# Kernel optimization log

Hardware: AMD Instinct MI355X
Metric: run time of the kernel (lower is better)

## Reference

```python
import jax, jax.numpy as jnp
import numpy as np

N, D_IN, F = 65536, 512, 256
E = 524288
BATCH, K1 = 32, 200
BN_EPS = 1e-5


def setup_inputs() -> dict:
    key = jax.random.key(0)
    ks = iter(jax.random.split(key, 64))

    def nrm(shape, s=0.05):
        return jax.random.normal(next(ks), shape, jnp.float32) * s

    inp = {
        "feat": jax.random.normal(next(ks), (N, D_IN), jnp.float32),
        "A": jax.random.randint(next(ks), (2, E), 0, N, dtype=jnp.int32),
        "h1id": jax.random.randint(next(ks), (BATCH * K1,), 0, N // BATCH, dtype=jnp.int32),
        "batch": BATCH,
    }
    dims = [(D_IN, F), (F, F), (F, F), (F, F)]
    for i, (di, do) in enumerate(dims, 1):
        inp[f"eps{i}"] = jnp.zeros((), jnp.float32)          # GINConv train_eps, init 0
        inp[f"w{i}a"] = nrm((di, do)); inp[f"b{i}a"] = jnp.zeros((do,), jnp.float32)
        inp[f"w{i}b"] = nrm((do, do)); inp[f"b{i}b"] = jnp.zeros((do,), jnp.float32)
        inp[f"g{i}"] = jnp.ones((do,), jnp.float32)          # BN gamma
        inp[f"be{i}"] = jnp.zeros((do,), jnp.float32)        # BN beta
        inp[f"m{i}"] = nrm((do,))                            # BN running mean
        inp[f"v{i}"] = jax.random.uniform(next(ks), (do,), jnp.float32, 0.5, 1.5)  # BN running var
    inp["wc1"] = nrm((F, F)); inp["bc1"] = jnp.zeros((F,), jnp.float32)
    inp["pa"] = jnp.full((F,), 0.25, jnp.float32)            # PReLU per-channel slope
    inp["wc2"] = nrm((F, 2)); inp["bc2"] = jnp.zeros((2,), jnp.float32)
    return inp


def _gin_conv(x, src, dst, eps, wa, ba, wb, bb, g, be, m, v):
    # sum aggregation over in-edges: aggr[i] = sum_{(j->i)} x[j]
    aggr = jax.ops.segment_sum(x[src], dst, num_segments=N)
    h = (1.0 + eps) * x + aggr
    h = jax.nn.relu(h @ wa + ba) @ wb + bb
    # BatchNorm1d in eval mode (running stats)
    return (h - m) * jax.lax.rsqrt(v + BN_EPS) * g + be


def _forward(feat, A, h1id, batch,
             eps1, w1a, b1a, w1b, b1b, g1, be1, m1, v1,
             eps2, w2a, b2a, w2b, b2b, g2, be2, m2, v2,
             eps3, w3a, b3a, w3b, b3b, g3, be3, m3, v3,
             eps4, w4a, b4a, w4b, b4b, g4, be4, m4, v4,
             wc1, bc1, pa, wc2, bc2):
    src, dst = A[0], A[1]
    h = jax.nn.relu(_gin_conv(feat, src, dst, eps1, w1a, b1a, w1b, b1b, g1, be1, m1, v1))
    h = jax.nn.relu(_gin_conv(h, src, dst, eps2, w2a, b2a, w2b, b2b, g2, be2, m2, v2))
    h = jax.nn.relu(_gin_conv(h, src, dst, eps3, w3a, b3a, w3b, b3b, g3, be3, m3, v3))
    h = _gin_conv(h, src, dst, eps4, w4a, b4a, w4b, b4b, g4, be4, m4, v4)
    score = h.reshape(batch, -1, F)                      # [B, n_per_graph, F]
    idx = h1id.reshape(batch, K1)
    edge_feat = jnp.take_along_axis(score, idx[:, :, None], axis=1)  # [B, K1, F]
    ef = edge_feat.reshape(-1, F)
    hc = ef @ wc1 + bc1
    hc = jnp.where(hc > 0, hc, pa * hc)                  # PReLU(256)
    return hc @ wc2 + bc2                                # [B*K1, 2]


def reference(feat, A, h1id, batch,
              eps1, w1a, b1a, w1b, b1b, g1, be1, m1, v1,
              eps2, w2a, b2a, w2b, b2b, g2, be2, m2, v2,
              eps3, w3a, b3a, w3b, b3b, g3, be3, m3, v3,
              eps4, w4a, b4a, w4b, b4b, g4, be4, m4, v4,
              wc1, bc1, pa, wc2, bc2):
    return _forward(feat, A, h1id, batch,
                    eps1, w1a, b1a, w1b, b1b, g1, be1, m1, v1,
                    eps2, w2a, b2a, w2b, b2b, g2, be2, m2, v2,
                    eps3, w3a, b3a, w3b, b3b, g3, be3, m3, v3,
                    eps4, w4a, b4a, w4b, b4b, g4, be4, m4, v4,
                    wc1, bc1, pa, wc2, bc2)
```

## Files before the change

kernel.cpp:

```cpp
#include <hip/hip_runtime.h>

typedef unsigned short u16;
typedef unsigned int   u32;
typedef __bf16  bf16x8 __attribute__((ext_vector_type(8)));
typedef float   f32x4  __attribute__((ext_vector_type(4)));
typedef u32     u32x4  __attribute__((ext_vector_type(4)));

#define NN 65536
#define NE 524288
#define FD 256

typedef const __attribute__((address_space(1))) void* gas_p;
typedef __attribute__((address_space(3))) void* las_p;
#define GLDS16(g, l) __builtin_amdgcn_global_load_lds((gas_p)(const void*)(g), (las_p)(void*)(l), 16, 0, 0)

__device__ __forceinline__ u16 f2bf(float f){
  u32 u = __float_as_uint(f);
  u += 0x7fffu + ((u >> 16) & 1u);
  return (u16)(u >> 16);
}
__device__ __forceinline__ float bf2f(u32 lo16){
  return __uint_as_float(lo16 << 16);
}
__device__ __forceinline__ void acc8(float* a, uint4 v){
  a[0] += bf2f(v.x & 0xffffu); a[1] += bf2f(v.x >> 16);
  a[2] += bf2f(v.y & 0xffffu); a[3] += bf2f(v.y >> 16);
  a[4] += bf2f(v.z & 0xffffu); a[5] += bf2f(v.z >> 16);
  a[6] += bf2f(v.w & 0xffffu); a[7] += bf2f(v.w >> 16);
}
__device__ __forceinline__ int lsw(int row, int c){
  return row * 256 + ((((c >> 3) ^ (row & 7)) & 31) << 3) + (c & 7);
}

__global__ __launch_bounds__(256) void prep_hist_k(
    const float* __restrict__ w1a, const float* __restrict__ w1b,
    const float* __restrict__ w2a, const float* __restrict__ w2b,
    const float* __restrict__ w3a, const float* __restrict__ w3b,
    const float* __restrict__ w4a, const float* __restrict__ w4b,
    const float* __restrict__ wc1, u16* __restrict__ wT,
    const int* __restrict__ dst, int* __restrict__ deg)
{
  if (blockIdx.x >= 2560){
    int e = (blockIdx.x - 2560) * 256 + threadIdx.x;
    atomicAdd(&deg[dst[e]], 1);
    return;
  }
  int idx = blockIdx.x * 256 + threadIdx.x;
  const float* src; int base, K, local;
  if (idx < 131072){ src = w1a; base = 0; K = 512; local = idx; }
  else {
    local = idx - 131072;
    int j = local >> 16;
    local &= 65535;
    K = 256;
    base = 131072 + j * 65536;
    switch (j){
      case 0: src = w1b; break;
      case 1: src = w2a; break;
      case 2: src = w2b; break;
      case 3: src = w3a; break;
      case 4: src = w3b; break;
      case 5: src = w4a; break;
      case 6: src = w4b; break;
      default: src = wc1; break;
    }
  }
  int n = local & 255;
  int k = local >> 8;
  wT[base + n * K + k] = f2bf(src[k * 256 + n]);
}

__global__ __launch_bounds__(1024) void scan_k(const int* __restrict__ deg, int* __restrict__ rs){
  __shared__ int part[1024];
  int t = threadIdx.x;
  int base = t * 64;
  int sum = 0;
  for (int i = 0; i < 64; ++i) sum += deg[base + i];
  part[t] = sum;
  __syncthreads();
  for (int off = 1; off < 1024; off <<= 1){
    int v = 0;
    if (t >= off) v = part[t - off];
    __syncthreads();
    part[t] += v;
    __syncthreads();
  }
  int run = part[t] - sum;
  for (int i = 0; i < 64; ++i){ rs[base + i] = run; run += deg[base + i]; }
  if (t == 1023) rs[65536] = part[1023];
}

__global__ __launch_bounds__(256) void scat_k(
    const int* __restrict__ src, const int* __restrict__ dst,
    const int* __restrict__ rs, int* __restrict__ cursor, int* __restrict__ csr)
{
  int e = blockIdx.x * 256 + threadIdx.x;
  int d = dst[e];
  int pos = atomicAdd(&cursor[d], 1);
  csr[rs[d] + pos] = src[e];
}

template<int AF32, int MODE, int RELU, int K>
__global__ __launch_bounds__(512) void gemm_k(
    const void* __restrict__ Ap, const u16* __restrict__ Bt,
    u16* __restrict__ C,
    const float* __restrict__ p0, const float* __restrict__ p1,
    const float* __restrict__ p2, const float* __restrict__ p3,
    const float* __restrict__ p4)
{
  __shared__ u16 lds[32768];
  u16* As = lds;
  u16* Bs = lds + 8192;
  const int t    = threadIdx.x;
  const int lane = t & 63;
  const int w    = t >> 6;
  const int wm   = w & 1;
  const int wn   = w >> 1;
  const int m0   = blockIdx.x * 128;
  const int mrow = lane & 15;
  const int quad = lane >> 4;

  f32x4 acc[4][4];
  const f32x4 zero = {0.f, 0.f, 0.f, 0.f};
  #pragma unroll
  for (int i = 0; i < 4; ++i)
    #pragma unroll
    for (int j = 0; j < 4; ++j) acc[i][j] = zero;

  const u16* Ab = (const u16*)Ap;
  const float* Af = (const float*)Ap;

  for (int k0 = 0; k0 < K; k0 += 64){
    if (AF32){
      #pragma unroll
      for (int i = 0; i < 2; ++i){
        int p   = i * 512 + t;
        int row = p >> 3;
        const float* s = Af + (size_t)(m0 + row) * K + k0 + (p & 7) * 8;
        float4 x0 = *(const float4*)s;
        float4 x1 = *(const float4*)(s + 4);
        union { u32x4 q; u16 h[8]; } u;
        u.h[0] = f2bf(x0.x); u.h[1] = f2bf(x0.y); u.h[2] = f2bf(x0.z); u.h[3] = f2bf(x0.w);
        u.h[4] = f2bf(x1.x); u.h[5] = f2bf(x1.y); u.h[6] = f2bf(x1.z); u.h[7] = f2bf(x1.w);
        int dst = (p & ~7) | ((p & 7) ^ (row & 7));
        *(u32x4*)&As[dst * 8] = u.q;
      }
    } else {
      #pragma unroll
      for (int i = 0; i < 2; ++i){
        int p   = i * 512 + t;
        int row = p >> 3;
        int ch  = (p & 7) ^ (row & 7);
        GLDS16(Ab + (size_t)(m0 + row) * K + k0 + ch * 8, &As[p * 8]);
      }
    }
    #pragma unroll
    for (int i = 0; i < 4; ++i){
      int p   = i * 512 + t;
      int row = p >> 3;
      int ch  = (p & 7) ^ (row & 7);
      GLDS16(Bt + (size_t)row * K + k0 + ch * 8, &Bs[p * 8]);
    }
    __syncthreads();
    #pragma unroll
    for (int ks = 0; ks < 2; ++ks){
      bf16x8 af[4], bq[4];
      #pragma unroll
      for (int mi = 0; mi < 4; ++mi){
        int r  = wm * 64 + mi * 16 + mrow;
        int ch = (quad + ks * 4) ^ (r & 7);
        af[mi] = *(const bf16x8*)&As[(r * 8 + ch) * 8];
      }
      #pragma unroll
      for (int ni = 0; ni < 4; ++ni){
        int rb = wn * 64 + ni * 16 + mrow;
        int ch = (quad + ks * 4) ^ (rb & 7);
        bq[ni] = *(const bf16x8*)&Bs[(rb * 8 + ch) * 8];
      }
      #pragma unroll
      for (int mi = 0; mi < 4; ++mi)
        #pragma unroll
        for (int ni = 0; ni < 4; ++ni)
          acc[mi][ni] = __builtin_amdgcn_mfma_f32_16x16x32_bf16(af[mi], bq[ni], acc[mi][ni], 0, 0, 0);
    }
    __syncthreads();
  }

  #pragma unroll
  for (int ni = 0; ni < 4; ++ni){
    int c  = wn * 64 + ni * 16 + mrow;
    float scale = 1.f, shift = 0.f;
    if (MODE == 1){
      float s = p0[c] * rsqrtf(p3[c] + 1e-5f);
      scale = s;
      shift = (p4[c] - p2[c]) * s + p1[c];
    }
    #pragma unroll
    for (int mi = 0; mi < 4; ++mi){
      int rbase = wm * 64 + mi * 16 + quad * 4;
      #pragma unroll
      for (int reg = 0; reg < 4; ++reg){
        float v = acc[mi][ni][reg];
        if (MODE == 1){
          v = v * scale + shift;
          if (RELU) v = fmaxf(v, 0.f);
        }
        lds[lsw(rbase + reg, c)] = f2bf(v);
      }
    }
  }
  __syncthreads();
  #pragma unroll
  for (int i = 0; i < 8; ++i){
    int p  = i * 512 + t;
    int r  = p >> 5;
    int ch = p & 31;
    u32x4 q = *(const u32x4*)&lds[r * 256 + (ch ^ (r & 7)) * 8];
    *(u32x4*)&C[(size_t)(m0 + r) * 256 + ch * 8] = q;
  }
}

template<int GATH, int RAW>
__global__ __launch_bounds__(256) void agg_k(
    const u16* __restrict__ y, const int* __restrict__ rs, const int* __restrict__ csr,
    const float* __restrict__ epsp, const float* __restrict__ bias,
    const int* __restrict__ gidx, u16* __restrict__ tout)
{
  int sub    = threadIdx.x >> 5;
  int lane32 = threadIdx.x & 31;
  int idx    = blockIdx.x * 8 + sub;
  int node;
  if (GATH) node = (idx / 200) * 2048 + gidx[idx];
  else      node = idx;
  int f0 = lane32 * 8;
  float e1 = 1.0f + epsp[0];
  int s0 = rs[node], s1 = rs[node + 1];
  uint4 own = *(const uint4*)(y + (size_t)node * 256 + f0);
  float a[8] = {0.f,0.f,0.f,0.f,0.f,0.f,0.f,0.f};
  int e = s0;
  for (; e + 4 <= s1; e += 4){
    int sa = csr[e], sb = csr[e+1], sc = csr[e+2], sd = csr[e+3];
    uint4 va = *(const uint4*)(y + (size_t)sa * 256 + f0);
    uint4 vb = *(const uint4*)(y + (size_t)sb * 256 + f0);
    uint4 vc = *(const uint4*)(y + (size_t)sc * 256 + f0);
    uint4 vd = *(const uint4*)(y + (size_t)sd * 256 + f0);
    acc8(a, va); acc8(a, vb); acc8(a, vc); acc8(a, vd);
  }
  for (; e < s1; ++e){
    int s = csr[e];
    acc8(a, *(const uint4*)(y + (size_t)s * 256 + f0));
  }
  float ow[8];
  ow[0] = bf2f(own.x & 0xffffu); ow[1] = bf2f(own.x >> 16);
  ow[2] = bf2f(own.y & 0xffffu); ow[3] = bf2f(own.y >> 16);
  ow[4] = bf2f(own.z & 0xffffu); ow[5] = bf2f(own.z >> 16);
  ow[6] = bf2f(own.w & 0xffffu); ow[7] = bf2f(own.w >> 16);
  float r[8];
  if (RAW){
    #pragma unroll
    for (int q = 0; q < 8; ++q) r[q] = e1 * ow[q] + a[q];
  } else {
    float4 b0 = *(const float4*)(bias + f0);
    float4 b1 = *(const float4*)(bias + f0 + 4);
    r[0] = fmaxf(e1 * ow[0] + a[0] + b0.x, 0.f);
    r[1] = fmaxf(e1 * ow[1] + a[1] + b0.y, 0.f);
    r[2] = fmaxf(e1 * ow[2] + a[2] + b0.z, 0.f);
    r[3] = fmaxf(e1 * ow[3] + a[3] + b0.w, 0.f);
    r[4] = fmaxf(e1 * ow[4] + a[4] + b1.x, 0.f);
    r[5] = fmaxf(e1 * ow[5] + a[5] + b1.y, 0.f);
    r[6] = fmaxf(e1 * ow[6] + a[6] + b1.z, 0.f);
    r[7] = fmaxf(e1 * ow[7] + a[7] + b1.w, 0.f);
  }
  uint4 o;
  o.x = (u32)f2bf(r[0]) | ((u32)f2bf(r[1]) << 16);
  o.y = (u32)f2bf(r[2]) | ((u32)f2bf(r[3]) << 16);
  o.z = (u32)f2bf(r[4]) | ((u32)f2bf(r[5]) << 16);
  o.w = (u32)f2bf(r[6]) | ((u32)f2bf(r[7]) << 16);
  *(uint4*)(tout + (size_t)idx * 256 + f0) = o;
}

__global__ __launch_bounds__(512) void tail_k(
    const u16* __restrict__ u4p, const u16* __restrict__ w4aT, const float* __restrict__ ba4,
    const u16* __restrict__ w4bT,
    const float* __restrict__ g, const float* __restrict__ be,
    const float* __restrict__ m, const float* __restrict__ v,
    const float* __restrict__ bb,
    const u16* __restrict__ wc1T, const float* __restrict__ bc1, const float* __restrict__ pa,
    const float* __restrict__ wc2, const float* __restrict__ bc2,
    float* __restrict__ out)
{
  __shared__ u16 lds[32768];
  const int t    = threadIdx.x;
  const int lane = t & 63;
  const int w    = t >> 6;
  const int wm   = w & 1;
  const int wn   = w >> 1;
  const int m0   = blockIdx.x * 128;
  const int mrow = lane & 15;
  const int quad = lane >> 4;
  const f32x4 zero = {0.f, 0.f, 0.f, 0.f};

  #pragma unroll
  for (int i = 0; i < 8; ++i){
    int p   = i * 512 + t;
    int row = p >> 5;
    int ch  = (p & 31) ^ (row & 7);
    GLDS16(u4p + (size_t)(m0 + row) * 256 + ch * 8, &lds[p * 8]);
  }
  __syncthreads();

  #pragma unroll 1
  for (int stage = 0; stage < 3; ++stage){
    const u16* Bt = (stage == 0) ? w4aT : (stage == 1) ? w4bT : wc1T;
    f32x4 acc[4][4];
    #pragma unroll
    for (int i = 0; i < 4; ++i)
      #pragma unroll
      for (int j = 0; j < 4; ++j) acc[i][j] = zero;
    #pragma unroll
    for (int ks = 0; ks < 8; ++ks){
      bf16x8 af[4], bq[4];
      #pragma unroll
      for (int mi = 0; mi < 4; ++mi){
        int r    = wm * 64 + mi * 16 + mrow;
        int slot = (ks * 4 + quad) ^ (r & 7);
        af[mi] = *(const bf16x8*)&lds[r * 256 + slot * 8];
      }
      #pragma unroll
      for (int ni = 0; ni < 4; ++ni){
        int rb = wn * 64 + ni * 16 + mrow;
        bq[ni] = *(const bf16x8*)&Bt[(size_t)rb * 256 + ks * 32 + quad * 8];
      }
      #pragma unroll
      for (int mi = 0; mi < 4; ++mi)
        #pragma unroll
        for (int ni = 0; ni < 4; ++ni)
          acc[mi][ni] = __builtin_amdgcn_mfma_f32_16x16x32_bf16(af[mi], bq[ni], acc[mi][ni], 0, 0, 0);
    }
    __syncthreads();
    #pragma unroll
    for (int ni = 0; ni < 4; ++ni){
      int c = wn * 64 + ni * 16 + mrow;
      float scale = 1.f, shift = 0.f, slope = 0.f; int prelu = 0, rel = 0;
      if (stage == 0){ shift = ba4[c]; rel = 1; }
      if (stage == 1){
        float s = g[c] * rsqrtf(v[c] + 1e-5f);
        scale = s;
        shift = (bb[c] - m[c]) * s + be[c];
      }
      if (stage == 2){ shift = bc1[c]; slope = pa[c]; prelu = 1; }
      #pragma unroll
      for (int mi = 0; mi < 4; ++mi){
        int rbase = wm * 64 + mi * 16 + quad * 4;
        #pragma unroll
        for (int reg = 0; reg < 4; ++reg){
          float val = acc[mi][ni][reg] * scale + shift;
          if (rel)   val = fmaxf(val, 0.f);
          if (prelu) val = val > 0.f ? val : slope * val;
          lds[lsw(rbase + reg, c)] = f2bf(val);
        }
      }
    }
    __syncthreads();
  }

  {
    int c0 = lane * 4;
    float4 wva = *(const float4*)(wc2 + c0 * 2);
    float4 wvb = *(const float4*)(wc2 + c0 * 2 + 4);
    float o0 = bc2[0], o1 = bc2[1];
    #pragma unroll 1
    for (int rr = 0; rr < 16; ++rr){
      int row = w * 16 + rr;
      int idxu = row * 256 + (((lane >> 1) ^ (row & 7)) << 3) + (c0 & 7);
      uint2 hv = *(const uint2*)&lds[idxu];
      float h0 = bf2f(hv.x & 0xffffu), h1 = bf2f(hv.x >> 16);
      float h2 = bf2f(hv.y & 0xffffu), h3 = bf2f(hv.y >> 16);
      float a0 = h0 * wva.x + h1 * wva.z + h2 * wvb.x + h3 * wvb.z;
      float a1 = h0 * wva.y + h1 * wva.w + h2 * wvb.y + h3 * wvb.w;
      #pragma unroll
      for (int off = 32; off > 0; off >>= 1){
        a0 += __shfl_xor(a0, off);
        a1 += __shfl_xor(a1, off);
      }
      if (lane == 0){
        out[(m0 + row) * 2]     = a0 + o0;
        out[(m0 + row) * 2 + 1] = a1 + o1;
      }
    }
  }
}

extern "C" void kernel_launch(void* const* d_in, const int* in_sizes, int n_in,
                              void* d_out, int out_size, void* d_ws, size_t ws_size,
                              hipStream_t stream)
{
  const float* feat = (const float*)d_in[0];
  const int*   A    = (const int*)d_in[1];
  const int*   h1id = (const int*)d_in[2];
  const float* eps[4] = {(const float*)d_in[4],  (const float*)d_in[13], (const float*)d_in[22], (const float*)d_in[31]};
  const float* wa [4] = {(const float*)d_in[5],  (const float*)d_in[14], (const float*)d_in[23], (const float*)d_in[32]};
  const float* ba [4] = {(const float*)d_in[6],  (const float*)d_in[15], (const float*)d_in[24], (const float*)d_in[33]};
  const float* wb [4] = {(const float*)d_in[7],  (const float*)d_in[16], (const float*)d_in[25], (const float*)d_in[34]};
  const float* bb [4] = {(const float*)d_in[8],  (const float*)d_in[17], (const float*)d_in[26], (const float*)d_in[35]};
  const float* g  [4] = {(const float*)d_in[9],  (const float*)d_in[18], (const float*)d_in[27], (const float*)d_in[36]};
  const float* be [4] = {(const float*)d_in[10], (const float*)d_in[19], (const float*)d_in[28], (const float*)d_in[37]};
  const float* m  [4] = {(const float*)d_in[11], (const float*)d_in[20], (const float*)d_in[29], (const float*)d_in[38]};
  const float* v  [4] = {(const float*)d_in[12], (const float*)d_in[21], (const float*)d_in[30], (const float*)d_in[39]};
  const float* wc1 = (const float*)d_in[40];
  const float* bc1 = (const float*)d_in[41];
  const float* pa  = (const float*)d_in[42];
  const float* wc2 = (const float*)d_in[43];
  const float* bc2 = (const float*)d_in[44];

  char* ws = (char*)d_ws;
  u16* wT     = (u16*)(ws + 0);
  int* deg    = (int*)(ws + 1310720);
  int* rs     = (int*)(ws + 1572864);
  int* cursor = (int*)(ws + 1835264);
  int* csr    = (int*)(ws + 2097408);
  u16* ybuf   = (u16*)(ws + 4194560);
  u16* tbuf   = (u16*)(ws + 37748992);
  u16* hbuf   = (u16*)(ws + 71303424);
  u16* u4     = (u16*)(ws + 104857856);

  u16* w1aT = wT;
  u16* w1bT = wT + 131072;
  u16* w2aT = wT + 196608;
  u16* w2bT = wT + 262144;
  u16* w3aT = wT + 327680;
  u16* w3bT = wT + 393216;
  u16* w4aT = wT + 458752;
  u16* w4bT = wT + 524288;
  u16* wc1T = wT + 589824;

  hipMemsetAsync(deg, 0, 65536 * 4, stream);
  hipMemsetAsync(cursor, 0, 65536 * 4, stream);
  prep_hist_k<<<4608, 256, 0, stream>>>(wa[0], wb[0], wa[1], wb[1], wa[2], wb[2],
      wa[3], wb[3], wc1, wT, A + NE, deg);
  scan_k<<<1, 1024, 0, stream>>>(deg, rs);
  scat_k<<<NE / 256, 256, 0, stream>>>(A, A + NE, rs, cursor, csr);

  gemm_k<1,0,0,512><<<512, 512, 0, stream>>>(feat, w1aT, ybuf,
      nullptr, nullptr, nullptr, nullptr, nullptr);
  agg_k<0,0><<<NN / 8, 256, 0, stream>>>(ybuf, rs, csr, eps[0], ba[0], nullptr, tbuf);
  gemm_k<0,1,1,256><<<512, 512, 0, stream>>>(tbuf, w1bT, hbuf,
      g[0], be[0], m[0], v[0], bb[0]);

  for (int l = 1; l <= 2; ++l){
    const u16* waT = (l == 1) ? w2aT : w3aT;
    const u16* wbT = (l == 1) ? w2bT : w3bT;
    gemm_k<0,0,0,256><<<512, 512, 0, stream>>>(hbuf, waT, ybuf,
        nullptr, nullptr, nullptr, nullptr, nullptr);
    agg_k<0,0><<<NN / 8, 256, 0, stream>>>(ybuf, rs, csr, eps[l], ba[l], nullptr, tbuf);
    gemm_k<0,1,1,256><<<512, 512, 0, stream>>>(tbuf, wbT, hbuf,
        g[l], be[l], m[l], v[l], bb[l]);
  }

  agg_k<1,1><<<800, 256, 0, stream>>>(hbuf, rs, csr, eps[3], nullptr, h1id, u4);
  tail_k<<<50, 512, 0, stream>>>(u4, w4aT, ba[3], w4bT,
      g[3], be[3], m[3], v[3], bb[3],
      wc1T, bc1, pa, wc2, bc2, (float*)d_out);

  (void)in_sizes; (void)n_in; (void)out_size; (void)ws_size;
}
```

Measured before the change: 650.2 us.

## Aggregate raw features first and fuse both MLP GEMMs for layers 2-3

For layers 2 and 3 the order changes from transform-then-aggregate to aggregate-then-transform, since the input and hidden widths are equal. A new dual_k kernel then runs both MLP GEMMs in one launch, keeping the intermediate ReLU activations in LDS instead of writing them to global memory. This removes one kernel launch and one intermediate round trip through global memory per layer. The second GEMM reads its weights straight from global memory without LDS staging, which may raise load latency, and the 64KB of LDS per block may limit occupancy.

```diff
diff --git a/kernel.cpp b/kernel.cpp
--- a/kernel.cpp
+++ b/kernel.cpp
@@ -206,6 +206,143 @@
           if (RELU) v = fmaxf(v, 0.f);
         }
         lds[lsw(rbase + reg, c)] = f2bf(v);
+      }
+    }
+  }
+  __syncthreads();
+  #pragma unroll
+  for (int i = 0; i < 8; ++i){
+    int p  = i * 512 + t;
+    int r  = p >> 5;
+    int ch = p & 31;
+    u32x4 q = *(const u32x4*)&lds[r * 256 + (ch ^ (r & 7)) * 8];
+    *(u32x4*)&C[(size_t)(m0 + r) * 256 + ch * 8] = q;
+  }
+}
+
+__global__ __launch_bounds__(512) void dual_k(
+    const u16* __restrict__ Up, const u16* __restrict__ B1t,
+    const float* __restrict__ ba,
+    const u16* __restrict__ B2t,
+    const float* __restrict__ g, const float* __restrict__ be,
+    const float* __restrict__ m, const float* __restrict__ v,
+    const float* __restrict__ bb,
+    u16* __restrict__ C)
+{
+  __shared__ u16 lds[32768];
+  u16* As = lds;
+  u16* Bs = lds + 8192;
+  const int t    = threadIdx.x;
+  const int lane = t & 63;
+  const int w    = t >> 6;
+  const int wm   = w & 1;
+  const int wn   = w >> 1;
+  const int m0   = blockIdx.x * 128;
+  const int mrow = lane & 15;
+  const int quad = lane >> 4;
+
+  const f32x4 zero = {0.f, 0.f, 0.f, 0.f};
+  f32x4 acc[4][4];
+  #pragma unroll
+  for (int i = 0; i < 4; ++i)
+    #pragma unroll
+    for (int j = 0; j < 4; ++j) acc[i][j] = zero;
+
+  for (int k0 = 0; k0 < 256; k0 += 64){
+    #pragma unroll
+    for (int i = 0; i < 2; ++i){
+      int p   = i * 512 + t;
+      int row = p >> 3;
+      int ch  = (p & 7) ^ (row & 7);
+      GLDS16(Up + (size_t)(m0 + row) * 256 + k0 + ch * 8, &As[p * 8]);
+    }
+    #pragma unroll
+    for (int i = 0; i < 4; ++i){
+      int p   = i * 512 + t;
+      int row = p >> 3;
+      int ch  = (p & 7) ^ (row & 7);
+      GLDS16(B1t + (size_t)row * 256 + k0 + ch * 8, &Bs[p * 8]);
+    }
+    __syncthreads();
+    #pragma unroll
+    for (int ks = 0; ks < 2; ++ks){
+      bf16x8 af[4], bq[4];
+      #pragma unroll
+      for (int mi = 0; mi < 4; ++mi){
+        int r  = wm * 64 + mi * 16 + mrow;
+        int ch = (quad + ks * 4) ^ (r & 7);
+        af[mi] = *(const bf16x8*)&As[(r * 8 + ch) * 8];
+      }
+      #pragma unroll
+      for (int ni = 0; ni < 4; ++ni){
+        int rb = wn * 64 + ni * 16 + mrow;
+        int ch = (quad + ks * 4) ^ (rb & 7);
+        bq[ni] = *(const bf16x8*)&Bs[(rb * 8 + ch) * 8];
+      }
+      #pragma unroll
+      for (int mi = 0; mi < 4; ++mi)
+        #pragma unroll
+        for (int ni = 0; ni < 4; ++ni)
+          acc[mi][ni] = __builtin_amdgcn_mfma_f32_16x16x32_bf16(af[mi], bq[ni], acc[mi][ni], 0, 0, 0);
+    }
+    __syncthreads();
+  }
+
+  #pragma unroll
+  for (int ni = 0; ni < 4; ++ni){
+    int c = wn * 64 + ni * 16 + mrow;
+    float shift = ba[c];
+    #pragma unroll
+    for (int mi = 0; mi < 4; ++mi){
+      int rbase = wm * 64 + mi * 16 + quad * 4;
+      #pragma unroll
+      for (int reg = 0; reg < 4; ++reg){
+        float val = fmaxf(acc[mi][ni][reg] + shift, 0.f);
+        lds[lsw(rbase + reg, c)] = f2bf(val);
+      }
+    }
+  }
+  __syncthreads();
+
+  f32x4 acc2[4][4];
+  #pragma unroll
+  for (int i = 0; i < 4; ++i)
+    #pragma unroll
+    for (int j = 0; j < 4; ++j) acc2[i][j] = zero;
+  #pragma unroll
+  for (int ks = 0; ks < 8; ++ks){
+    bf16x8 af[4], bq[4];
+    #pragma unroll
+    for (int mi = 0; mi < 4; ++mi){
+      int r    = wm * 64 + mi * 16 + mrow;
+      int slot = (ks * 4 + quad) ^ (r & 7);
+      af[mi] = *(const bf16x8*)&lds[r * 256 + slot * 8];
+    }
+    #pragma unroll
+    for (int ni = 0; ni < 4; ++ni){
+      int rb = wn * 64 + ni * 16 + mrow;
+      bq[ni] = *(const bf16x8*)&B2t[(size_t)rb * 256 + ks * 32 + quad * 8];
+    }
+    #pragma unroll
+    for (int mi = 0; mi < 4; ++mi)
+      #pragma unroll
+      for (int ni = 0; ni < 4; ++ni)
+        acc2[mi][ni] = __builtin_amdgcn_mfma_f32_16x16x32_bf16(af[mi], bq[ni], acc2[mi][ni], 0, 0, 0);
+  }
+  __syncthreads();
+
+  #pragma unroll
+  for (int ni = 0; ni < 4; ++ni){
+    int c = wn * 64 + ni * 16 + mrow;
+    float scale = g[c] * rsqrtf(v[c] + 1e-5f);
+    float shift = (bb[c] - m[c]) * scale + be[c];
+    #pragma unroll
+    for (int mi = 0; mi < 4; ++mi){
+      int rbase = wm * 64 + mi * 16 + quad * 4;
+      #pragma unroll
+      for (int reg = 0; reg < 4; ++reg){
+        float val = fmaxf(acc2[mi][ni][reg] * scale + shift, 0.f);
+        lds[lsw(rbase + reg, c)] = f2bf(val);
       }
     }
   }
@@ -447,15 +584,12 @@
   gemm_k<0,1,1,256><<<512, 512, 0, stream>>>(tbuf, w1bT, hbuf,
       g[0], be[0], m[0], v[0], bb[0]);
 
-  for (int l = 1; l <= 2; ++l){
-    const u16* waT = (l == 1) ? w2aT : w3aT;
-    const u16* wbT = (l == 1) ? w2bT : w3bT;
-    gemm_k<0,0,0,256><<<512, 512, 0, stream>>>(hbuf, waT, ybuf,
-        nullptr, nullptr, nullptr, nullptr, nullptr);
-    agg_k<0,0><<<NN / 8, 256, 0, stream>>>(ybuf, rs, csr, eps[l], ba[l], nullptr, tbuf);
-    gemm_k<0,1,1,256><<<512, 512, 0, stream>>>(tbuf, wbT, hbuf,
-        g[l], be[l], m[l], v[l], bb[l]);
-  }
+  agg_k<0,1><<<NN / 8, 256, 0, stream>>>(hbuf, rs, csr, eps[1], nullptr, nullptr, ybuf);
+  dual_k<<<512, 512, 0, stream>>>(ybuf, w2aT, ba[1], w2bT,
+      g[1], be[1], m[1], v[1], bb[1], hbuf);
+  agg_k<0,1><<<NN / 8, 256, 0, stream>>>(hbuf, rs, csr, eps[2], nullptr, nullptr, ybuf);
+  dual_k<<<512, 512, 0, stream>>>(ybuf, w3aT, ba[2], w3bT,
+      g[2], be[2], m[2], v[2], bb[2], hbuf);
 
   agg_k<1,1><<<800, 256, 0, stream>>>(hbuf, rs, csr, eps[3], nullptr, h1id, u4);
   tail_k<<<50, 512, 0, stream>>>(u4, w4aT, ba[3], w4bT,
```

After: 645.2 us. No clear change (-0.8%).

## Split GEMM into 128x128 tiles, fuse scatter with layer-1 GEMM, reorder layers 2-3

Applied to the files above, without the earlier changes.

The GEMM kernel is retiled from 128x256 per 512-thread block to 128x128 per 256-thread block, which doubles the grid and halves LDS use per block to raise occupancy. The CSR scatter is merged into the first GEMM launch as extra blocks, so it runs alongside the matmul instead of as a separate serialized kernel. Layers 2 and 3 now aggregate raw features before the first linear layer, with a new MODE 3 that adds bias and applies ReLU, in place of transform-then-aggregate. The reordering is algebraically equivalent, but it trades kernel fusion and the old bias placement for a different epilogue, and the smaller tiles reload the A operand twice.

```diff
diff --git a/kernel.cpp b/kernel.cpp
--- a/kernel.cpp
+++ b/kernel.cpp
@@ -90,25 +90,15 @@
   if (t == 1023) rs[65536] = part[1023];
 }
 
-__global__ __launch_bounds__(256) void scat_k(
-    const int* __restrict__ src, const int* __restrict__ dst,
-    const int* __restrict__ rs, int* __restrict__ cursor, int* __restrict__ csr)
-{
-  int e = blockIdx.x * 256 + threadIdx.x;
-  int d = dst[e];
-  int pos = atomicAdd(&cursor[d], 1);
-  csr[rs[d] + pos] = src[e];
-}
-
 template<int AF32, int MODE, int RELU, int K>
-__global__ __launch_bounds__(512) void gemm_k(
+__device__ __forceinline__ void gemm_body(
+    u16* lds, int bid,
     const void* __restrict__ Ap, const u16* __restrict__ Bt,
     u16* __restrict__ C,
     const float* __restrict__ p0, const float* __restrict__ p1,
     const float* __restrict__ p2, const float* __restrict__ p3,
     const float* __restrict__ p4)
 {
-  __shared__ u16 lds[32768];
   u16* As = lds;
   u16* Bs = lds + 8192;
   const int t    = threadIdx.x;
@@ -116,7 +106,8 @@
   const int w    = t >> 6;
   const int wm   = w & 1;
   const int wn   = w >> 1;
-  const int m0   = blockIdx.x * 128;
+  const int m0   = (bid >> 1) * 128;
+  const int n0   = (bid & 1) * 128;
   const int mrow = lane & 15;
   const int quad = lane >> 4;
 
@@ -133,22 +124,22 @@
   for (int k0 = 0; k0 < K; k0 += 64){
     if (AF32){
       #pragma unroll
-      for (int i = 0; i < 2; ++i){
-        int p   = i * 512 + t;
+      for (int i = 0; i < 4; ++i){
+        int p   = i * 256 + t;
         int row = p >> 3;
-        const float* s = Af + (size_t)(m0 + row) * K + k0 + (p & 7) * 8;
+        int ch  = (p & 7) ^ (row & 7);
+        const float* s = Af + (size_t)(m0 + row) * K + k0 + ch * 8;
         float4 x0 = *(const float4*)s;
         float4 x1 = *(const float4*)(s + 4);
         union { u32x4 q; u16 h[8]; } u;
         u.h[0] = f2bf(x0.x); u.h[1] = f2bf(x0.y); u.h[2] = f2bf(x0.z); u.h[3] = f2bf(x0.w);
         u.h[4] = f2bf(x1.x); u.h[5] = f2bf(x1.y); u.h[6] = f2bf(x1.z); u.h[7] = f2bf(x1.w);
-        int dst = (p & ~7) | ((p & 7) ^ (row & 7));
-        *(u32x4*)&As[dst * 8] = u.q;
+        *(u32x4*)&As[p * 8] = u.q;
       }
     } else {
       #pragma unroll
-      for (int i = 0; i < 2; ++i){
-        int p   = i * 512 + t;
+      for (int i = 0; i < 4; ++i){
+        int p   = i * 256 + t;
         int row = p >> 3;
         int ch  = (p & 7) ^ (row & 7);
         GLDS16(Ab + (size_t)(m0 + row) * K + k0 + ch * 8, &As[p * 8]);
@@ -156,10 +147,10 @@
     }
     #pragma unroll
     for (int i = 0; i < 4; ++i){
-      int p   = i * 512 + t;
+      int p   = i * 256 + t;
       int row = p >> 3;
       int ch  = (p & 7) ^ (row & 7);
-      GLDS16(Bt + (size_t)row * K + k0 + ch * 8, &Bs[p * 8]);
+      GLDS16(Bt + (size_t)(n0 + row) * K + k0 + ch * 8, &Bs[p * 8]);
     }
     __syncthreads();
     #pragma unroll
@@ -188,36 +179,72 @@
 
   #pragma unroll
   for (int ni = 0; ni < 4; ++ni){
-    int c  = wn * 64 + ni * 16 + mrow;
+    int cl = wn * 64 + ni * 16 + mrow;
+    int c  = n0 + cl;
     float scale = 1.f, shift = 0.f;
     if (MODE == 1){
       float s = p0[c] * rsqrtf(p3[c] + 1e-5f);
       scale = s;
       shift = (p4[c] - p2[c]) * s + p1[c];
     }
+    if (MODE == 3){ shift = p0[c]; }
     #pragma unroll
     for (int mi = 0; mi < 4; ++mi){
       int rbase = wm * 64 + mi * 16 + quad * 4;
       #pragma unroll
       for (int reg = 0; reg < 4; ++reg){
+        int row = rbase + reg;
         float v = acc[mi][ni][reg];
         if (MODE == 1){
           v = v * scale + shift;
           if (RELU) v = fmaxf(v, 0.f);
         }
-        lds[lsw(rbase + reg, c)] = f2bf(v);
+        if (MODE == 3){
+          v = fmaxf(v + shift, 0.f);
+        }
+        lds[row * 128 + (((cl >> 3) ^ (row & 7)) << 3) + (cl & 7)] = f2bf(v);
       }
     }
   }
   __syncthreads();
   #pragma unroll
   for (int i = 0; i < 8; ++i){
-    int p  = i * 512 + t;
-    int r  = p >> 5;
-    int ch = p & 31;
-    u32x4 q = *(const u32x4*)&lds[r * 256 + (ch ^ (r & 7)) * 8];
-    *(u32x4*)&C[(size_t)(m0 + r) * 256 + ch * 8] = q;
-  }
+    int p  = i * 256 + t;
+    int r  = p >> 4;
+    int ch = p & 15;
+    u32x4 q = *(const u32x4*)&lds[r * 128 + ((ch ^ (r & 7)) << 3)];
+    *(u32x4*)&C[(size_t)(m0 + r) * 256 + n0 + ch * 8] = q;
+  }
+}
+
+template<int AF32, int MODE, int RELU, int K>
+__global__ __launch_bounds__(256) void gemm_k(
+    const void* __restrict__ Ap, const u16* __restrict__ Bt,
+    u16* __restrict__ C,
+    const float* __restrict__ p0, const float* __restrict__ p1,
+    const float* __restrict__ p2, const float* __restrict__ p3,
+    const float* __restrict__ p4)
+{
+  __shared__ u16 lds[16384];
+  gemm_body<AF32, MODE, RELU, K>(lds, blockIdx.x, Ap, Bt, C, p0, p1, p2, p3, p4);
+}
+
+__global__ __launch_bounds__(256) void gemm1_scat_k(
+    const float* __restrict__ Af, const u16* __restrict__ Bt,
+    u16* __restrict__ C,
+    const int* __restrict__ esrc, const int* __restrict__ edst,
+    const int* __restrict__ rs, int* __restrict__ cursor, int* __restrict__ csr)
+{
+  __shared__ u16 lds[16384];
+  if (blockIdx.x >= 1024){
+    int e = (blockIdx.x - 1024) * 256 + threadIdx.x;
+    int d = edst[e];
+    int pos = atomicAdd(&cursor[d], 1);
+    csr[rs[d] + pos] = esrc[e];
+    return;
+  }
+  gemm_body<1, 0, 0, 512>(lds, blockIdx.x, Af, Bt, C,
+      nullptr, nullptr, nullptr, nullptr, nullptr);
 }
 
 template<int GATH, int RAW>
@@ -439,23 +466,24 @@
   prep_hist_k<<<4608, 256, 0, stream>>>(wa[0], wb[0], wa[1], wb[1], wa[2], wb[2],
       wa[3], wb[3], wc1, wT, A + NE, deg);
   scan_k<<<1, 1024, 0, stream>>>(deg, rs);
-  scat_k<<<NE / 256, 256, 0, stream>>>(A, A + NE, rs, cursor, csr);
-
-  gemm_k<1,0,0,512><<<512, 512, 0, stream>>>(feat, w1aT, ybuf,
-      nullptr, nullptr, nullptr, nullptr, nullptr);
+
+  gemm1_scat_k<<<3072, 256, 0, stream>>>(feat, w1aT, ybuf,
+      A, A + NE, rs, cursor, csr);
+
   agg_k<0,0><<<NN / 8, 256, 0, stream>>>(ybuf, rs, csr, eps[0], ba[0], nullptr, tbuf);
-  gemm_k<0,1,1,256><<<512, 512, 0, stream>>>(tbuf, w1bT, hbuf,
+  gemm_k<0,1,1,256><<<1024, 256, 0, stream>>>(tbuf, w1bT, hbuf,
       g[0], be[0], m[0], v[0], bb[0]);
 
-  for (int l = 1; l <= 2; ++l){
-    const u16* waT = (l == 1) ? w2aT : w3aT;
-    const u16* wbT = (l == 1) ? w2bT : w3bT;
-    gemm_k<0,0,0,256><<<512, 512, 0, stream>>>(hbuf, waT, ybuf,
-        nullptr, nullptr, nullptr, nullptr, nullptr);
-    agg_k<0,0><<<NN / 8, 256, 0, stream>>>(ybuf, rs, csr, eps[l], ba[l], nullptr, tbuf);
-    gemm_k<0,1,1,256><<<512, 512, 0, stream>>>(tbuf, wbT, hbuf,
-        g[l], be[l], m[l], v[l], bb[l]);
-  }
+  agg_k<0,1><<<NN / 8, 256, 0, stream>>>(hbuf, rs, csr, eps[1], nullptr, nullptr, ybuf);
+  gemm_k<0,3,0,256><<<1024, 256, 0, stream>>>(ybuf, w2aT, tbuf,
+      ba[1], nullptr, nullptr, nullptr, nullptr);
+  gemm_k<0,1,1,256><<<1024, 256, 0, stream>>>(tbuf, w2bT, hbuf,
+      g[1], be[1], m[1], v[1], bb[1]);
+  agg_k<0,1><<<NN / 8, 256, 0, stream>>>(hbuf, rs, csr, eps[2], nullptr, nullptr, ybuf);
+  gemm_k<0,3,0,256><<<1024, 256, 0, stream>>>(ybuf, w3aT, tbuf,
+      ba[2], nullptr, nullptr, nullptr, nullptr);
+  gemm_k<0,1,1,256><<<1024, 256, 0, stream>>>(tbuf, w3bT, hbuf,
+      g[2], be[2], m[2], v[2], bb[2]);
 
   agg_k<1,1><<<800, 256, 0, stream>>>(hbuf, rs, csr, eps[3], nullptr, h1id, u4);
   tail_k<<<50, 512, 0, stream>>>(u4, w4aT, ba[3], w4bT,
```

After: 645.6 us. Within noise of the previous version (-0.7%).
